# Kernel tuning notes

Hardware: AMD Instinct MI355X
Metric: run time of the kernel (lower is better)

## Reference

```python
import jax, jax.numpy as jnp
import numpy as np

N = 50000
D = 128
E = 600000
C = 128  # out_channels


def setup_inputs() -> dict:
    key = jax.random.key(0)
    ks = jax.random.split(key, 8)
    x = jax.random.normal(ks[0], (N, D), dtype=jnp.float32)
    edge_index = jax.random.randint(ks[1], (2, E), 0, N, dtype=jnp.int64)
    s = 1.0 / np.sqrt(D)
    # layer 1: PyG GraphConv = lin_rel (with bias) on aggregated neighbors + lin_root (no bias) on self
    W1_rel = jax.random.uniform(ks[2], (C, D), jnp.float32, -s, s)
    b1_rel = jax.random.uniform(ks[3], (C,), jnp.float32, -s, s)
    W1_root = jax.random.uniform(ks[4], (C, D), jnp.float32, -s, s)
    s2 = 1.0 / np.sqrt(C)
    W2_rel = jax.random.uniform(ks[5], (C, C), jnp.float32, -s2, s2)
    b2_rel = jax.random.uniform(ks[6], (C,), jnp.float32, -s2, s2)
    W2_root = jax.random.uniform(ks[7], (C, C), jnp.float32, -s2, s2)
    return {"x": x, "edge_index": edge_index,
            "W1_rel": W1_rel, "b1_rel": b1_rel, "W1_root": W1_root,
            "W2_rel": W2_rel, "b2_rel": b2_rel, "W2_root": W2_root}


def _graph_conv(x, src, tgt, W_rel, b_rel, W_root):
    # sum-aggregate source-node features onto targets, then linear transforms
    agg = jax.ops.segment_sum(x[src], tgt, num_segments=N)  # [N, d_in]
    return agg @ W_rel.T + b_rel + x @ W_root.T


def reference(x, edge_index, W1_rel, b1_rel, W1_root, W2_rel, b2_rel, W2_root):
    src, tgt = edge_index[0], edge_index[1]
    h = jax.nn.relu(_graph_conv(x, src, tgt, W1_rel, b1_rel, W1_root))
    h = jax.nn.relu(_graph_conv(h, src, tgt, W2_rel, b2_rel, W2_root))
    return h
```

## Files before the change

kernel.cpp:

```cpp
#include <hip/hip_runtime.h>
#include <hip/hip_bf16.h>

#define DD 128
#define STRIDE 32
#define BINSZ 4096
#define EPB 2048

typedef __attribute__((ext_vector_type(8))) short bf16x8;
typedef __attribute__((ext_vector_type(4))) float f32x4;
typedef __attribute__((ext_vector_type(8))) unsigned short us8;
typedef __attribute__((ext_vector_type(4))) unsigned short us4;
typedef unsigned short ushort_t;
typedef unsigned int uint_t;

__device__ inline ushort_t f2bf(float f) {
    __hip_bfloat16 h = __float2bfloat16(f);
    union { __hip_bfloat16 h; ushort_t u; } cv;
    cv.h = h;
    return cv.u;
}
__device__ inline float bf2f(uint_t lo16) {
    union { uint_t i; float f; } v;
    v.i = lo16 << 16;
    return v.f;
}
__device__ inline void conv8(const float* __restrict__ in, ushort_t* __restrict__ outp) {
    const float4 va = *(const float4*)in;
    const float4 vb = *(const float4*)(in + 4);
    ushort_t r[8];
    r[0] = f2bf(va.x); r[1] = f2bf(va.y); r[2] = f2bf(va.z); r[3] = f2bf(va.w);
    r[4] = f2bf(vb.x); r[5] = f2bf(vb.y); r[6] = f2bf(vb.z); r[7] = f2bf(vb.w);
    *(bf16x8*)outp = *(bf16x8*)r;
}


__global__ __launch_bounds__(256) void prep_small(int* __restrict__ binCursor,
                                                  ushort_t* __restrict__ xb,
                                                  ushort_t* __restrict__ aggb, int n) {
    const int t = threadIdx.x;
    binCursor[t] = 0;
    if (t < 64)       ((uint_t*)(xb + (size_t)n * DD))[t] = 0u;
    if (t >= 64 && t < 128) ((uint_t*)(aggb + (size_t)n * DD))[t - 64] = 0u;
    if (t >= 128 && t < 192) ((uint_t*)(xb + (size_t)n * DD))[t - 128 + 0] = 0u;
}


__global__ __launch_bounds__(256) void bin_scatter_conv(
    const int* __restrict__ tgt, const int* __restrict__ src,
    int* __restrict__ binCursor, uint_t* __restrict__ binReg, int e, int eb,
    const float* __restrict__ x, ushort_t* __restrict__ xb, int n8, int xcb,
    const float* __restrict__ a, const float* __restrict__ b,
    const float* __restrict__ c, const float* __restrict__ d,
    ushort_t* __restrict__ wb)
{
    const int blk = blockIdx.x;
    if (blk < eb) {
        __shared__ int lcnt[256];
        __shared__ int lbase[256];
        const int tid = threadIdx.x;
        lcnt[tid] = 0;
        __syncthreads();

        const int ebase = blk * EPB + tid * 8;
        const bool valid = (ebase + 8 <= e);
        int tg[8], sr[8], bn[8];
        if (valid) {
            int4 t0 = ((const int4*)tgt)[ebase / 4];
            int4 t1 = ((const int4*)tgt)[ebase / 4 + 1];
            int4 s0 = ((const int4*)src)[ebase / 4];
            int4 s1 = ((const int4*)src)[ebase / 4 + 1];
            tg[0] = t0.x; tg[1] = t0.y; tg[2] = t0.z; tg[3] = t0.w;
            tg[4] = t1.x; tg[5] = t1.y; tg[6] = t1.z; tg[7] = t1.w;
            sr[0] = s0.x; sr[1] = s0.y; sr[2] = s0.z; sr[3] = s0.w;
            sr[4] = s1.x; sr[5] = s1.y; sr[6] = s1.z; sr[7] = s1.w;
#pragma unroll
            for (int k = 0; k < 8; ++k) {
                bn[k] = tg[k] >> 8;
                atomicAdd(&lcnt[bn[k]], 1);
            }
        }
        __syncthreads();
        {
            int c0 = lcnt[tid];
            int gb = (c0 > 0) ? atomicAdd(&binCursor[tid], c0) : 0;
            lbase[tid] = gb;
            lcnt[tid] = 0;
        }
        __syncthreads();
        if (valid) {
#pragma unroll
            for (int k = 0; k < 8; ++k) {
                int r = atomicAdd(&lcnt[bn[k]], 1);
                int slot = lbase[bn[k]] + r;
                if (slot > BINSZ - 1) slot = BINSZ - 1;
                binReg[(size_t)bn[k] * BINSZ + slot] =
                    ((uint_t)(tg[k] & 255) << 16) | (uint_t)sr[k];
            }
        }
        if (blk == 0 && tid == 0) {
            for (int j = e & ~7; j < e; ++j) {
                int t = tgt[j], b2 = t >> 8;
                int slot = atomicAdd(&binCursor[b2], 1);
                if (slot > BINSZ - 1) slot = BINSZ - 1;
                binReg[(size_t)b2 * BINSZ + slot] =
                    ((uint_t)(t & 255) << 16) | (uint_t)src[j];
            }
        }
    } else if (blk < eb + xcb) {
        int i = (blk - eb) * 256 + threadIdx.x;
        if (i < n8) conv8(x + (size_t)i * 8, xb + (size_t)i * 8);
    } else {
        int k = (blk - eb - xcb) * 256 + threadIdx.x;
        if (k >= 8192) return;
        const float* p = (k < 2048) ? a : (k < 4096) ? b : (k < 6144) ? c : d;
        conv8(p + (size_t)(k & 2047) * 8, wb + (size_t)k * 8);
    }
}


__global__ __launch_bounds__(256) void bin_finalize(const int* __restrict__ binCursor,
                                                    const uint_t* __restrict__ binReg,
                                                    ushort_t* __restrict__ esrc,
                                                    int* __restrict__ pos, int n) {
    const int bin = blockIdx.x;
    const int tid = threadIdx.x;
    __shared__ int cnt[256];
    __shared__ __align__(16) ushort_t lbkt[256 * STRIDE];
    cnt[tid] = 0;
    us8 f;
#pragma unroll
    for (int k = 0; k < 8; ++k) f[k] = (ushort_t)n;
    for (int i = tid; i < 256 * STRIDE / 8; i += 256) ((us8*)lbkt)[i] = f;
    __syncthreads();
    int total = binCursor[bin];
    if (total > BINSZ) total = BINSZ;
    const uint_t* reg = binReg + (size_t)bin * BINSZ;
    for (int i = tid; i < total; i += 256) {
        uint_t p = reg[i];
        int node = p >> 16;
        int r = atomicAdd(&cnt[node], 1) & (STRIDE - 1);
        lbkt[node * STRIDE + r] = (ushort_t)(p & 0xffffu);
    }
    __syncthreads();
    us8* g = (us8*)(esrc + (size_t)bin * 256 * STRIDE);
    for (int i = tid; i < 256 * STRIDE / 8; i += 256) g[i] = ((us8*)lbkt)[i];
    int node = bin * 256 + tid;
    if (node < n) {
        int dg = cnt[tid];
        pos[node] = dg > STRIDE ? STRIDE : dg;
    }
}


__device__ __forceinline__ void gather_body(int bid, int tid,
                                            const ushort_t* __restrict__ xin,
                                            const int* __restrict__ pos,
                                            const ushort_t* __restrict__ esrc,
                                            ushort_t* __restrict__ agg,
                                            int node_lo, int node_hi) {
    const int lane = tid & 63;
    const int node = node_lo + bid * 4 + (tid >> 6);
    if (node >= node_hi) return;
    int deg = pos[node];
    deg = deg > STRIDE ? STRIDE : deg;
    const int epochs = (deg + 15) >> 4;
    const int grp = lane >> 4;
    const int l16 = lane & 15;
    const ushort_t* bktg = esrc + (size_t)node * STRIDE + grp * 4;
    const ushort_t* xcol = xin + l16 * 8;
    float acc[8];
#pragma unroll
    for (int c = 0; c < 8; ++c) acc[c] = 0.f;

    for (int ep = 0; ep < epochs; ++ep) {
        us4 idv = *(const us4*)(bktg + ep * 16);
        bf16x8 v0 = *(const bf16x8*)(xcol + (size_t)idv[0] * DD);
        bf16x8 v1 = *(const bf16x8*)(xcol + (size_t)idv[1] * DD);
        bf16x8 v2 = *(const bf16x8*)(xcol + (size_t)idv[2] * DD);
        bf16x8 v3 = *(const bf16x8*)(xcol + (size_t)idv[3] * DD);
#pragma unroll
        for (int c = 0; c < 8; ++c) {
            acc[c] += bf2f((ushort_t)v0[c]) + bf2f((ushort_t)v1[c])
                    + bf2f((ushort_t)v2[c]) + bf2f((ushort_t)v3[c]);
        }
    }
#pragma unroll
    for (int c = 0; c < 8; ++c) {
        acc[c] += __shfl_xor(acc[c], 16, 64);
        acc[c] += __shfl_xor(acc[c], 32, 64);
    }
    if (lane < 16) {
        ushort_t r[8];
#pragma unroll
        for (int c = 0; c < 8; ++c) r[c] = f2bf(acc[c]);
        *(bf16x8*)(agg + (size_t)node * DD + l16 * 8) = *(bf16x8*)r;
    }
}


template<bool OUT_BF16>
__device__ __forceinline__ void gemm_body(int bid, int tid,
                                          const ushort_t* Aagg, const ushort_t* __restrict__ Aroot,
                                          const ushort_t* __restrict__ Wrel,
                                          const ushort_t* __restrict__ Wroot,
                                          const float* __restrict__ bias, void* outv,
                                          int row_lo, int row_hi) {
    const int wave = tid >> 6;
    const int lane = tid & 63;
    const int m = lane & 15;
    const int kg = lane >> 4;
    const int rbase = row_lo + bid * 64 + wave * 16;
    if (rbase >= row_hi) return;
    const size_t aoff = (size_t)(rbase + m) * DD + kg * 8;

    f32x4 acc[8];
#pragma unroll
    for (int j = 0; j < 8; ++j) acc[j] = (f32x4){0.f, 0.f, 0.f, 0.f};

#pragma unroll
    for (int k0 = 0; k0 < DD; k0 += 32) {
        bf16x8 aA = *(const bf16x8*)(Aagg + aoff + k0);
        bf16x8 aR = *(const bf16x8*)(Aroot + aoff + k0);
#pragma unroll
        for (int j = 0; j < 8; ++j) {
            bf16x8 bL = *(const bf16x8*)(Wrel + (size_t)(j * 16 + m) * DD + kg * 8 + k0);
            bf16x8 bR = *(const bf16x8*)(Wroot + (size_t)(j * 16 + m) * DD + kg * 8 + k0);
            acc[j] = __builtin_amdgcn_mfma_f32_16x16x32_bf16(aA, bL, acc[j], 0, 0, 0);
            acc[j] = __builtin_amdgcn_mfma_f32_16x16x32_bf16(aR, bR, acc[j], 0, 0, 0);
        }
    }

    const int orow = rbase + kg * 4;
#pragma unroll
    for (int j = 0; j < 8; ++j) {
        const int col = j * 16 + m;
        const float bv = bias[col];
#pragma unroll
        for (int i = 0; i < 4; ++i) {
            float v = acc[j][i] + bv;
            v = v > 0.f ? v : 0.f;
            if (OUT_BF16)
                ((ushort_t*)outv)[(size_t)(orow + i) * DD + col] = f2bf(v);
            else
                ((float*)outv)[(size_t)(orow + i) * DD + col] = v;
        }
    }
}


__global__ __launch_bounds__(256) void gather_k(const ushort_t* __restrict__ xin,
                                                const int* __restrict__ pos,
                                                const ushort_t* __restrict__ esrc,
                                                ushort_t* __restrict__ agg, int lo, int hi) {
    gather_body(blockIdx.x, threadIdx.x, xin, pos, esrc, agg, lo, hi);
}

template<bool OUT_BF16>
__global__ __launch_bounds__(256) void gemm_k(const ushort_t* Aagg, const ushort_t* Aroot,
                                              const ushort_t* Wrel, const ushort_t* Wroot,
                                              const float* bias, void* outv, int lo, int hi) {
    gemm_body<OUT_BF16>(blockIdx.x, threadIdx.x, Aagg, Aroot, Wrel, Wroot, bias, outv, lo, hi);
}

template<bool OUT_BF16>
__global__ __launch_bounds__(256) void gg_k(const ushort_t* Aagg, const ushort_t* Aroot,
                                            const ushort_t* Wrel, const ushort_t* Wroot,
                                            const float* bias, void* outv, int glo, int ghi,
                                            const ushort_t* xin, const int* pos,
                                            const ushort_t* esrc, ushort_t* agg,
                                            int alo, int ahi, int gemmBlocks) {
    if ((int)blockIdx.x < gemmBlocks)
        gemm_body<OUT_BF16>(blockIdx.x, threadIdx.x, Aagg, Aroot, Wrel, Wroot, bias, outv, glo, ghi);
    else
        gather_body(blockIdx.x - gemmBlocks, threadIdx.x, xin, pos, esrc, agg, alo, ahi);
}

extern "C" void kernel_launch(void* const* d_in, const int* in_sizes, int n_in,
                              void* d_out, int out_size, void* d_ws, size_t ws_size,
                              hipStream_t stream) {
    const float* x = (const float*)d_in[0];
    const int* ei = (const int*)d_in[1];
    const float* W1rel = (const float*)d_in[2];
    const float* b1 = (const float*)d_in[3];
    const float* W1root = (const float*)d_in[4];
    const float* W2rel = (const float*)d_in[5];
    const float* b2 = (const float*)d_in[6];
    const float* W2root = (const float*)d_in[7];
    float* out = (float*)d_out;

    const int n = in_sizes[0] / DD;
    const int e = in_sizes[1] / 2;
    const int* src = ei;
    const int* tgt = ei + e;
    const int n8 = n * DD / 8;
    const int xcb = (n8 + 255) / 256;
    const int eb = (e + EPB - 1) / EPB;
    const int nbins = (n + 255) >> 8;

    const int NHA = 24960;
    const int gbA = NHA / 64;
    const int gbB = (n - NHA + 63) / 64;
    const int agA = NHA / 4;
    const int agB = (n - NHA + 3) / 4;

    char* ws = (char*)d_ws;
    int* pos = (int*)ws;
    int* binCursor = (int*)(ws + 200064);
    ushort_t* wb = (ushort_t*)(ws + 201088);
    ushort_t* esrc = (ushort_t*)(ws + 332160);
    uint_t* binReg = (uint_t*)(ws + 3543424);
    ushort_t* aggb = (ushort_t*)(ws + 6754816);
    ushort_t* xb = (ushort_t*)(ws + 19555072);

    prep_small<<<1, 256, 0, stream>>>(binCursor, xb, aggb, n);
    bin_scatter_conv<<<eb + xcb + 32, 256, 0, stream>>>(
        tgt, src, binCursor, binReg, e, eb, x, xb, n8, xcb,
        W1rel, W1root, W2rel, W2root, wb);
    bin_finalize<<<nbins, 256, 0, stream>>>(binCursor, binReg, esrc, pos, n);

    gather_k<<<agA, 256, 0, stream>>>(xb, pos, esrc, aggb, 0, NHA);
    gg_k<true><<<gbA + agB, 256, 0, stream>>>(
        aggb, xb, wb, wb + 16384, b1, aggb, 0, NHA,
        xb, pos, esrc, aggb, NHA, n, gbA);
    gemm_k<true><<<gbB, 256, 0, stream>>>(aggb, xb, wb, wb + 16384, b1, aggb, NHA, n);

    gather_k<<<agA, 256, 0, stream>>>(aggb, pos, esrc, xb, 0, NHA);
    gg_k<false><<<gbA + agB, 256, 0, stream>>>(
        xb, aggb, wb + 32768, wb + 49152, b2, out, 0, NHA,
        aggb, pos, esrc, xb, NHA, n, gbA);
    gemm_k<false><<<gbB, 256, 0, stream>>>(xb, aggb, wb + 32768, wb + 49152, b2, out, NHA, n);
}
```

Baseline: 155.2 us.

## Prefill edge buckets in prep kernel and interleave gemm/gather blocks

The padding fill of the per-node source-index buckets moves out of bin_finalize into the prep kernel, which now runs many blocks. bin_finalize then writes each edge straight to global memory instead of staging 16 KB in shared memory and copying it out. The combined gemm+gather kernel now spreads gemm blocks evenly among gather blocks (one every P), so both workloads share the GPU over the whole launch instead of running as two separate phases. The cost is scattered 2-byte global writes in finalize, and workspace offsets shift slightly.

```diff
diff --git a/kernel.cpp b/kernel.cpp
--- a/kernel.cpp
+++ b/kernel.cpp
@@ -34,14 +34,26 @@
 }
 
 
-__global__ __launch_bounds__(256) void prep_small(int* __restrict__ binCursor,
+__global__ __launch_bounds__(256) void prep_small(ushort_t* __restrict__ esrc, int pb,
+                                                  int* __restrict__ binCursor,
                                                   ushort_t* __restrict__ xb,
                                                   ushort_t* __restrict__ aggb, int n) {
-    const int t = threadIdx.x;
-    binCursor[t] = 0;
-    if (t < 64)       ((uint_t*)(xb + (size_t)n * DD))[t] = 0u;
-    if (t >= 64 && t < 128) ((uint_t*)(aggb + (size_t)n * DD))[t - 64] = 0u;
-    if (t >= 128 && t < 192) ((uint_t*)(xb + (size_t)n * DD))[t - 128 + 0] = 0u;
+    const int blk = blockIdx.x;
+    if (blk < pb) {
+        int i = blk * 256 + threadIdx.x;
+        if (i < n * (STRIDE / 8)) {
+            us8 f;
+#pragma unroll
+            for (int k = 0; k < 8; ++k) f[k] = (ushort_t)n;
+            ((us8*)esrc)[i] = f;
+        }
+    } else if (blk == pb) {
+        binCursor[threadIdx.x] = 0;
+    } else {
+        int t = threadIdx.x;
+        if (t < 64)       ((uint_t*)(xb + (size_t)n * DD))[t] = 0u;
+        else if (t < 128) ((uint_t*)(aggb + (size_t)n * DD))[t - 64] = 0u;
+    }
 }
 
 
@@ -125,12 +137,7 @@
     const int bin = blockIdx.x;
     const int tid = threadIdx.x;
     __shared__ int cnt[256];
-    __shared__ __align__(16) ushort_t lbkt[256 * STRIDE];
     cnt[tid] = 0;
-    us8 f;
-#pragma unroll
-    for (int k = 0; k < 8; ++k) f[k] = (ushort_t)n;
-    for (int i = tid; i < 256 * STRIDE / 8; i += 256) ((us8*)lbkt)[i] = f;
     __syncthreads();
     int total = binCursor[bin];
     if (total > BINSZ) total = BINSZ;
@@ -139,11 +146,9 @@
         uint_t p = reg[i];
         int node = p >> 16;
         int r = atomicAdd(&cnt[node], 1) & (STRIDE - 1);
-        lbkt[node * STRIDE + r] = (ushort_t)(p & 0xffffu);
+        esrc[(size_t)(bin * 256 + node) * STRIDE + r] = (ushort_t)(p & 0xffffu);
     }
     __syncthreads();
-    us8* g = (us8*)(esrc + (size_t)bin * 256 * STRIDE);
-    for (int i = tid; i < 256 * STRIDE / 8; i += 256) g[i] = ((us8*)lbkt)[i];
     int node = bin * 256 + tid;
     if (node < n) {
         int dg = cnt[tid];
@@ -268,11 +273,16 @@
                                             const float* bias, void* outv, int glo, int ghi,
                                             const ushort_t* xin, const int* pos,
                                             const ushort_t* esrc, ushort_t* agg,
-                                            int alo, int ahi, int gemmBlocks) {
-    if ((int)blockIdx.x < gemmBlocks)
-        gemm_body<OUT_BF16>(blockIdx.x, threadIdx.x, Aagg, Aroot, Wrel, Wroot, bias, outv, glo, ghi);
-    else
-        gather_body(blockIdx.x - gemmBlocks, threadIdx.x, xin, pos, esrc, agg, alo, ahi);
+                                            int alo, int ahi, int gemmBlocks, int P) {
+    const int bid = blockIdx.x;
+    const int q = bid / P;
+    if ((bid % P) == 0 && q < gemmBlocks) {
+        gemm_body<OUT_BF16>(q, threadIdx.x, Aagg, Aroot, Wrel, Wroot, bias, outv, glo, ghi);
+    } else {
+        int before = (bid + P - 1) / P;
+        if (before > gemmBlocks) before = gemmBlocks;
+        gather_body(bid - before, threadIdx.x, xin, pos, esrc, agg, alo, ahi);
+    }
 }
 
 extern "C" void kernel_launch(void* const* d_in, const int* in_sizes, int n_in,
@@ -294,6 +304,7 @@
     const int* tgt = ei + e;
     const int n8 = n * DD / 8;
     const int xcb = (n8 + 255) / 256;
+    const int pb = (n * (STRIDE / 8) + 255) / 256;
     const int eb = (e + EPB - 1) / EPB;
     const int nbins = (n + 255) >> 8;
 
@@ -302,31 +313,33 @@
     const int gbB = (n - NHA + 63) / 64;
     const int agA = NHA / 4;
     const int agB = (n - NHA + 3) / 4;
+    const int T = gbA + agB;
+    const int P = T / gbA;
 
     char* ws = (char*)d_ws;
     int* pos = (int*)ws;
     int* binCursor = (int*)(ws + 200064);
     ushort_t* wb = (ushort_t*)(ws + 201088);
     ushort_t* esrc = (ushort_t*)(ws + 332160);
-    uint_t* binReg = (uint_t*)(ws + 3543424);
-    ushort_t* aggb = (ushort_t*)(ws + 6754816);
-    ushort_t* xb = (ushort_t*)(ws + 19555072);
-
-    prep_small<<<1, 256, 0, stream>>>(binCursor, xb, aggb, n);
+    uint_t* binReg = (uint_t*)(ws + 3532160);
+    ushort_t* aggb = (ushort_t*)(ws + 6743424);
+    ushort_t* xb = (ushort_t*)(ws + 19543680);
+
+    prep_small<<<pb + 2, 256, 0, stream>>>(esrc, pb, binCursor, xb, aggb, n);
     bin_scatter_conv<<<eb + xcb + 32, 256, 0, stream>>>(
         tgt, src, binCursor, binReg, e, eb, x, xb, n8, xcb,
         W1rel, W1root, W2rel, W2root, wb);
     bin_finalize<<<nbins, 256, 0, stream>>>(binCursor, binReg, esrc, pos, n);
 
     gather_k<<<agA, 256, 0, stream>>>(xb, pos, esrc, aggb, 0, NHA);
-    gg_k<true><<<gbA + agB, 256, 0, stream>>>(
+    gg_k<true><<<T, 256, 0, stream>>>(
         aggb, xb, wb, wb + 16384, b1, aggb, 0, NHA,
-        xb, pos, esrc, aggb, NHA, n, gbA);
+        xb, pos, esrc, aggb, NHA, n, gbA, P);
     gemm_k<true><<<gbB, 256, 0, stream>>>(aggb, xb, wb, wb + 16384, b1, aggb, NHA, n);
 
     gather_k<<<agA, 256, 0, stream>>>(aggb, pos, esrc, xb, 0, NHA);
-    gg_k<false><<<gbA + agB, 256, 0, stream>>>(
+    gg_k<false><<<T, 256, 0, stream>>>(
         xb, aggb, wb + 32768, wb + 49152, b2, out, 0, NHA,
-        aggb, pos, esrc, xb, NHA, n, gbA);
+        aggb, pos, esrc, xb, NHA, n, gbA, P);
     gemm_k<false><<<gbB, 256, 0, stream>>>(xb, aggb, wb + 32768, wb + 49152, b2, out, NHA, n);
 }
```

New measurement: 174.5 us. 1.12x slower.
